# Performance work log

Hardware: AMD Instinct MI355X
Metric: run time of the kernel (lower is better)

The kernel has to match this reference:

```python
import jax, jax.numpy as jnp
import numpy as np

SHIFT = 1  # fixed value of the randomized self.shift_direction (+1 or -1)


def _unfold_h3(t):
    """torch.nn.functional.unfold with kernel (3,1), padding (1,0),
    returned as (N, C, 3, H, W) patches (channel-major, kernel-minor order,
    matching torch's C*kh*kw channel layout)."""
    n, c, h, w = t.shape
    tp = jnp.pad(t, ((0, 0), (0, 0), (1, 1), (0, 0)))
    return jnp.stack([tp[:, :, k:k + h, :] for k in range(3)], axis=2)


def setup_inputs() -> dict:
    key = jax.random.key(0)
    kx, k1, k2 = jax.random.split(key, 3)
    x = jax.random.normal(kx, (128, 128, 56, 56), dtype=jnp.float32)
    w1 = jax.random.normal(k1, (64, 3, 4), dtype=jnp.float32)
    w2 = jax.random.normal(k2, (2, 3, 32), dtype=jnp.float32)
    return {"x": x, "w1": w1, "w2": w2}


def reference(x, w1, w2):
    # channel-group shift along H
    t = x.reshape(128, 64, 2, 56, 56)
    t = jnp.roll(t, SHIFT, axis=3)
    t = t.reshape(128, 128, 56, 56)
    # stage 1: vertical 3-tap patches + contraction over (k=64 channels, i=3 taps)
    p = _unfold_h3(t).reshape(128, 64, 2, 3, 56, 56)   # l k n i m o
    t4 = jnp.einsum('lknimo,kij->lnmoj', p, w1)        # (128, 2, 56, 56, 4)
    # stage 2: fold (n,m)->112 channels, 3-tap patches along o-dim, contract (i=2, k=3)
    t5 = t4.reshape(128, 112, 56, 4)
    p2 = _unfold_h3(t5).reshape(128, 2, 56, 3, 56, 4)  # l i m k n o
    t6 = jnp.einsum('limkno,ikj->lmnoj', p2, w2)       # (128, 56, 56, 4, 32)
    y = jnp.transpose(t6, (0, 1, 2, 4, 3)).reshape(128, 56, 56, 128)
    return jnp.transpose(y, (0, 3, 1, 2))              # (128, 128, 56, 56)
```

## Files before the change

### kernel.cpp

```cpp
#include <hip/hip_runtime.h>


__global__ __launch_bounds__(448) void stage1_kernel(
    const float* __restrict__ x, const float* __restrict__ w1,
    float* __restrict__ t4)
{
    const int l = blockIdx.x / 7;
    const int p = (blockIdx.x % 7) * 448 + threadIdx.x;
    const int m = p / 56;
    const int o = p - m * 56;

    int   off[3];
    bool  valid[3];
#pragma unroll
    for (int t = 0; t < 3; ++t) {
        const int h = m + t - 1;
        valid[t] = (h >= 0) && (h < 56);
        const int row = (h <= 0) ? 55 : (h - 1);
        off[t] = row * 56 + o;
    }

    float acc[2][4];
#pragma unroll
    for (int i2 = 0; i2 < 2; ++i2)
#pragma unroll
        for (int j = 0; j < 4; ++j) acc[i2][j] = 0.0f;

    const float* xl = x + (size_t)l * 128 * 3136;

    for (int k = 0; k < 64; ++k) {
        float w[3][4];
#pragma unroll
        for (int t = 0; t < 3; ++t)
#pragma unroll
            for (int j = 0; j < 4; ++j)
                w[t][j] = w1[(k * 3 + t) * 4 + j];

#pragma unroll
        for (int i2 = 0; i2 < 2; ++i2) {
            const float* xc = xl + (size_t)(2 * k + i2) * 3136;
#pragma unroll
            for (int t = 0; t < 3; ++t) {
                const float xv = valid[t] ? xc[off[t]] : 0.0f;
#pragma unroll
                for (int j = 0; j < 4; ++j)
                    acc[i2][j] = fmaf(xv, w[t][j], acc[i2][j]);
            }
        }
    }

    float* t4l = t4 + (size_t)l * 8 * 3136 + p;
#pragma unroll
    for (int i2 = 0; i2 < 2; ++i2)
#pragma unroll
        for (int j = 0; j < 4; ++j)
            t4l[(size_t)(i2 * 4 + j) * 3136] = acc[i2][j];
}

__global__ __launch_bounds__(256) void stage2_kernel(
    const float* __restrict__ t4, const float* __restrict__ w2,
    float* __restrict__ out)
{
    const int l = blockIdx.x / 56;
    const int m = blockIdx.x % 56;

    __shared__ float lds[8 * 58];
    const int tid = threadIdx.x;

    if (tid < 16) lds[(tid >> 1) * 58 + (tid & 1) * 57] = 0.0f;
    for (int t = tid; t < 448; t += 256) {
        const int io = t / 56;
        const int np = t - io * 56;
        lds[io * 58 + 1 + np] =
            t4[((size_t)l * 8 + io) * 3136 + m * 56 + np];
    }
    __syncthreads();

    const int n  = tid & 63;
    const int o4 = tid >> 6;
    if (n >= 56) return;

    float v[2][3];
#pragma unroll
    for (int i = 0; i < 2; ++i)
#pragma unroll
        for (int k = 0; k < 3; ++k)
            v[i][k] = lds[(i * 4 + o4) * 58 + n + k];

    float* ob = out + (((size_t)l * 128 + o4) * 56 + m) * 56 + n;

#pragma unroll
    for (int j = 0; j < 32; ++j) {
        float s = 0.0f;
#pragma unroll
        for (int i = 0; i < 2; ++i)
#pragma unroll
            for (int k = 0; k < 3; ++k)
                s = fmaf(v[i][k], w2[(i * 3 + k) * 32 + j], s);
        ob[(size_t)(j * 4) * 3136] = s;
    }
}

extern "C" void kernel_launch(void* const* d_in, const int* in_sizes, int n_in,
                              void* d_out, int out_size, void* d_ws, size_t ws_size,
                              hipStream_t stream)
{
    const float* x  = (const float*)d_in[0];
    const float* w1 = (const float*)d_in[1];
    const float* w2 = (const float*)d_in[2];
    float* out = (float*)d_out;
    float* t4  = (float*)d_ws;

    stage1_kernel<<<dim3(128 * 7), dim3(448), 0, stream>>>(x, w1, t4);
    stage2_kernel<<<dim3(128 * 56), dim3(256), 0, stream>>>(t4, w2, out);
}
```

Baseline: 385.4 us.

## Vectorize both stages with float4 per-thread tiles and remap grids

Stage 1 now has each thread compute four adjacent output columns, using float4 loads of x and float4 stores of t4. The boundary check moves into the weights as a multiplier, so the loads carry no branch. Blocks are remapped across 392 blocks with an XCD-style interleave. Stage 2 now stages half-image planes of t4 into LDS and writes four contiguous outputs per thread with float4 stores, where the old version wrote scattered scalars. This cuts the memory instruction count, but the smaller grid of stage 1 (392 blocks of 256) may reduce occupancy, and the register use per thread grows.

```diff
diff --git a/kernel.cpp b/kernel.cpp
--- a/kernel.cpp
+++ b/kernel.cpp
@@ -1,32 +1,29 @@
 #include <hip/hip_runtime.h>
 
 
-__global__ __launch_bounds__(448) void stage1_kernel(
+__global__ __launch_bounds__(256) void stage1_kernel(
     const float* __restrict__ x, const float* __restrict__ w1,
     float* __restrict__ t4)
 {
-    const int l = blockIdx.x / 7;
-    const int p = (blockIdx.x % 7) * 448 + threadIdx.x;
-    const int m = p / 56;
-    const int o = p - m * 56;
+    const int bid  = (blockIdx.x & 7) * 49 + (blockIdx.x >> 3);
+    const int item = bid * 256 + threadIdx.x;
+    const int l  = item / 784;
+    const int r  = item - l * 784;
+    const int m  = r / 14;
+    const int o0 = (r - m * 14) * 4;
 
     int   off[3];
-    bool  valid[3];
+    float vf[3];
 #pragma unroll
     for (int t = 0; t < 3; ++t) {
         const int h = m + t - 1;
-        valid[t] = (h >= 0) && (h < 56);
+        vf[t] = (h >= 0 && h < 56) ? 1.0f : 0.0f;
         const int row = (h <= 0) ? 55 : (h - 1);
-        off[t] = row * 56 + o;
+        off[t] = row * 56 + o0;
     }
 
-    float acc[2][4];
-#pragma unroll
-    for (int i2 = 0; i2 < 2; ++i2)
-#pragma unroll
-        for (int j = 0; j < 4; ++j) acc[i2][j] = 0.0f;
-
-    const float* xl = x + (size_t)l * 128 * 3136;
+    float acc[2][4][4] = {};
+    const float* xl = x + (size_t)l * (128 * 3136);
 
     for (int k = 0; k < 64; ++k) {
         float w[3][4];
@@ -34,70 +31,88 @@
         for (int t = 0; t < 3; ++t)
 #pragma unroll
             for (int j = 0; j < 4; ++j)
-                w[t][j] = w1[(k * 3 + t) * 4 + j];
+                w[t][j] = w1[(k * 3 + t) * 4 + j] * vf[t];
 
 #pragma unroll
         for (int i2 = 0; i2 < 2; ++i2) {
             const float* xc = xl + (size_t)(2 * k + i2) * 3136;
 #pragma unroll
             for (int t = 0; t < 3; ++t) {
-                const float xv = valid[t] ? xc[off[t]] : 0.0f;
+                const float4 xv = *reinterpret_cast<const float4*>(xc + off[t]);
 #pragma unroll
-                for (int j = 0; j < 4; ++j)
-                    acc[i2][j] = fmaf(xv, w[t][j], acc[i2][j]);
+                for (int j = 0; j < 4; ++j) {
+                    acc[i2][j][0] = fmaf(xv.x, w[t][j], acc[i2][j][0]);
+                    acc[i2][j][1] = fmaf(xv.y, w[t][j], acc[i2][j][1]);
+                    acc[i2][j][2] = fmaf(xv.z, w[t][j], acc[i2][j][2]);
+                    acc[i2][j][3] = fmaf(xv.w, w[t][j], acc[i2][j][3]);
+                }
             }
         }
     }
 
-    float* t4l = t4 + (size_t)l * 8 * 3136 + p;
+    float* tp = t4 + (size_t)l * (8 * 3136) + m * 56 + o0;
 #pragma unroll
     for (int i2 = 0; i2 < 2; ++i2)
 #pragma unroll
-        for (int j = 0; j < 4; ++j)
-            t4l[(size_t)(i2 * 4 + j) * 3136] = acc[i2][j];
+        for (int j = 0; j < 4; ++j) {
+            const float4 v = make_float4(acc[i2][j][0], acc[i2][j][1],
+                                         acc[i2][j][2], acc[i2][j][3]);
+            *reinterpret_cast<float4*>(tp + (size_t)(i2 * 4 + j) * 3136) = v;
+        }
 }
 
 __global__ __launch_bounds__(256) void stage2_kernel(
     const float* __restrict__ t4, const float* __restrict__ w2,
     float* __restrict__ out)
 {
-    const int l = blockIdx.x / 56;
-    const int m = blockIdx.x % 56;
+    const int l  = blockIdx.x >> 3;
+    const int o4 = (blockIdx.x >> 1) & 3;
+    const int mh = blockIdx.x & 1;
 
-    __shared__ float lds[8 * 58];
+    __shared__ float lds[2][1568];
     const int tid = threadIdx.x;
 
-    if (tid < 16) lds[(tid >> 1) * 58 + (tid & 1) * 57] = 0.0f;
-    for (int t = tid; t < 448; t += 256) {
-        const int io = t / 56;
-        const int np = t - io * 56;
-        lds[io * 58 + 1 + np] =
-            t4[((size_t)l * 8 + io) * 3136 + m * 56 + np];
+    const float* p0 = t4 + ((size_t)l * 8 + 0 + o4) * 3136 + mh * 1568;
+    const float* p1 = t4 + ((size_t)l * 8 + 4 + o4) * 3136 + mh * 1568;
+    for (int t = tid; t < 784; t += 256) {
+        const int i2 = (t >= 392);
+        const int p4 = i2 ? t - 392 : t;
+        const float4 v = *reinterpret_cast<const float4*>(
+            (i2 ? p1 : p0) + (size_t)p4 * 4);
+        *reinterpret_cast<float4*>(&lds[i2][p4 * 4]) = v;
     }
     __syncthreads();
 
-    const int n  = tid & 63;
-    const int o4 = tid >> 6;
-    if (n >= 56) return;
+    for (int ch = tid; ch < 392; ch += 256) {
+        const int ml = ch / 14;
+        const int n0 = (ch - ml * 14) * 4;
+        const int m  = mh * 28 + ml;
 
-    float v[2][3];
-#pragma unroll
-    for (int i = 0; i < 2; ++i)
-#pragma unroll
-        for (int k = 0; k < 3; ++k)
-            v[i][k] = lds[(i * 4 + o4) * 58 + n + k];
-
-    float* ob = out + (((size_t)l * 128 + o4) * 56 + m) * 56 + n;
-
-#pragma unroll
-    for (int j = 0; j < 32; ++j) {
-        float s = 0.0f;
+        float tv[2][6];
 #pragma unroll
         for (int i = 0; i < 2; ++i)
 #pragma unroll
-            for (int k = 0; k < 3; ++k)
-                s = fmaf(v[i][k], w2[(i * 3 + k) * 32 + j], s);
-        ob[(size_t)(j * 4) * 3136] = s;
+            for (int d = 0; d < 6; ++d) {
+                const int nn = n0 - 1 + d;
+                tv[i][d] = (nn >= 0 && nn < 56) ? lds[i][ml * 56 + nn] : 0.0f;
+            }
+
+        float* ob = out + ((size_t)l * 128 + o4) * 3136 + m * 56 + n0;
+#pragma unroll
+        for (int j = 0; j < 32; ++j) {
+            float4 s = make_float4(0.f, 0.f, 0.f, 0.f);
+#pragma unroll
+            for (int i = 0; i < 2; ++i)
+#pragma unroll
+                for (int k = 0; k < 3; ++k) {
+                    const float wv = w2[(i * 3 + k) * 32 + j];
+                    s.x = fmaf(tv[i][k + 0], wv, s.x);
+                    s.y = fmaf(tv[i][k + 1], wv, s.y);
+                    s.z = fmaf(tv[i][k + 2], wv, s.z);
+                    s.w = fmaf(tv[i][k + 3], wv, s.w);
+                }
+            *reinterpret_cast<float4*>(ob + (size_t)j * 4 * 3136) = s;
+        }
     }
 }
 
@@ -111,6 +126,6 @@
     float* out = (float*)d_out;
     float* t4  = (float*)d_ws;
 
-    stage1_kernel<<<dim3(128 * 7), dim3(448), 0, stream>>>(x, w1, t4);
-    stage2_kernel<<<dim3(128 * 56), dim3(256), 0, stream>>>(t4, w2, out);
+    stage1_kernel<<<dim3(392), dim3(256), 0, stream>>>(x, w1, t4);
+    stage2_kernel<<<dim3(1024), dim3(256), 0, stream>>>(t4, w2, out);
 }
```

Result: slower. 439.4 us (+14.0%).
